# Kernel optimization log

Hardware: AMD Instinct MI355X
Metric: run time of the kernel (lower is better)

The kernel has to match this reference:

```python
import jax, jax.numpy as jnp
import numpy as np

N_SRC = 100000
N_EDGES = 1000000
IN_FEATS = 64
N_CLASSES = 64


def setup_inputs() -> dict:
    key = jax.random.key(0)
    k1, k2, k3, k4, k5 = jax.random.split(key, 5)
    x = jax.random.normal(k1, (N_SRC, IN_FEATS), dtype=jnp.float32)
    W_self = jax.random.normal(k2, (IN_FEATS, N_CLASSES), dtype=jnp.float32) / np.sqrt(IN_FEATS)
    W_neigh = jax.random.normal(k3, (IN_FEATS, N_CLASSES), dtype=jnp.float32) / np.sqrt(IN_FEATS)
    b = jnp.zeros((N_CLASSES,), dtype=jnp.float32)
    src = jax.random.randint(k4, (N_EDGES,), 0, N_SRC, dtype=jnp.int32)
    dst = jax.random.randint(k5, (N_EDGES,), 0, N_SRC, dtype=jnp.int32)
    return {"x": x, "W_self": W_self, "W_neigh": W_neigh, "b": b,
            "src": src, "dst": dst, "num_dst": N_SRC}


def reference(x, W_self, W_neigh, b, src, dst, num_dst):
    # SAGEConv 'mean': gather src features along edges, segment-mean into dst,
    # then rst = h_dst @ W_self + h_neigh_mean @ W_neigh + b, followed by relu.
    msgs = x[src]                                                   # [E, F] irregular gather
    summed = jax.ops.segment_sum(msgs, dst, num_segments=num_dst)   # [num_dst, F]
    deg = jax.ops.segment_sum(jnp.ones((src.shape[0],), x.dtype), dst,
                              num_segments=num_dst)                 # [num_dst]
    h_neigh = summed / jnp.maximum(deg, 1.0)[:, None]               # mean (0 for isolated)
    h_dst = x[:num_dst]
    h = h_dst @ W_self + h_neigh @ W_neigh + b
    return jax.nn.relu(h)
```

## Files before the change

### kernel.cpp

```cpp
#include <hip/hip_runtime.h>


constexpr int F = 64;
constexpr int BROWS = 256;
constexpr int MAXNB = 512;
constexpr int CHP = 4096;
constexpr int SCAP = 2048;
constexpr int LDH = 72;

typedef __attribute__((ext_vector_type(8))) short short8;
typedef __attribute__((ext_vector_type(4))) float float4v;

__device__ inline unsigned short f2bf(float f) {
    union { float f; unsigned u; } c; c.f = f;
    unsigned u = c.u;
    return (unsigned short)((u + 0x7FFFu + ((u >> 16) & 1u)) >> 16);
}
__device__ inline float bf2f(unsigned short h) {
    union { unsigned u; float f; } c; c.u = (unsigned)h << 16;
    return c.f;
}

__global__ __launch_bounds__(256) void k_conv(const float* __restrict__ x,
                                              const float* __restrict__ Ws,
                                              const float* __restrict__ Wn,
                                              unsigned short* __restrict__ xb,
                                              unsigned short* __restrict__ WtG,
                                              const int* __restrict__ dst,
                                              int* __restrict__ cnt,
                                              long n4, int n_edges, int nchunk) {
    __shared__ int hist[MAXNB];
    int t = threadIdx.x;
    long tid = (long)blockIdx.x * 256 + t;
    if (tid < 2 * F * F) {
        int i = (int)tid;
        int n = i & 63, k = i >> 6;
        float v = (k < 64) ? Ws[k * 64 + n] : Wn[(k - 64) * 64 + n];
        WtG[n * 128 + k] = f2bf(v);
    }
    int c = blockIdx.x;
    if (c < nchunk) {
        for (int i = t; i < MAXNB; i += 256) hist[i] = 0;
        __syncthreads();
        int e0 = c * CHP, e1 = min(e0 + CHP, n_edges);
        for (int e = e0 + t; e < e1; e += 256) atomicAdd(&hist[dst[e] >> 8], 1);
        __syncthreads();
        for (int i = t; i < MAXNB; i += 256) cnt[(long)c * MAXNB + i] = hist[i];
    }
    for (long i = tid; i < n4; i += (long)gridDim.x * 256) {
        float4 v = ((const float4*)x)[i];
        ushort4 o;
        o.x = f2bf(v.x); o.y = f2bf(v.y); o.z = f2bf(v.z); o.w = f2bf(v.w);
        ((ushort4*)xb)[i] = o;
    }
}

__global__ __launch_bounds__(512) void k_scanA(int* __restrict__ cnt,
                                               int* __restrict__ btot, int nchunk) {
    int b = (blockIdx.x * 512 + threadIdx.x) >> 6;
    int lane = threadIdx.x & 63;
    if (b >= MAXNB) return;
    int per = (nchunk + 63) / 64;
    int c0 = lane * per;
    int vals[16];
    int lsum = 0;
#pragma unroll
    for (int i = 0; i < 16; ++i) {
        if (i < per) {
            int c = c0 + i;
            int v = (c < nchunk) ? cnt[(long)c * MAXNB + b] : 0;
            vals[i] = v; lsum += v;
        }
    }
    int incl = lsum;
    for (int off = 1; off < 64; off <<= 1) {
        int o = __shfl_up(incl, off);
        if (lane >= off) incl += o;
    }
    int run = incl - lsum;
#pragma unroll
    for (int i = 0; i < 16; ++i) {
        if (i < per) {
            int c = c0 + i;
            if (c < nchunk) { cnt[(long)c * MAXNB + b] = run; run += vals[i]; }
        }
    }
    int tot = __shfl(incl, 63);
    if (lane == 0) btot[b] = tot;
}

__global__ __launch_bounds__(512) void k_scanB(const int* __restrict__ btot,
                                               int* __restrict__ bstart) {
    __shared__ int wtot[8];
    __shared__ int woff[8];
    int t = threadIdx.x;
    int lane = t & 63, wave = t >> 6;
    int v = btot[t];
    int incl = v;
    for (int off = 1; off < 64; off <<= 1) {
        int o = __shfl_up(incl, off);
        if (lane >= off) incl += o;
    }
    if (lane == 63) wtot[wave] = incl;
    __syncthreads();
    if (t == 0) { int s = 0; for (int i = 0; i < 8; ++i) { woff[i] = s; s += wtot[i]; } }
    __syncthreads();
    bstart[t] = incl - v + woff[wave];
    if (t == 511) bstart[MAXNB] = woff[7] + incl;
}

__global__ __launch_bounds__(512) void k_place(const int* __restrict__ src,
                                               const int* __restrict__ dst,
                                               const int* __restrict__ cnt,
                                               const int* __restrict__ bstart,
                                               unsigned* __restrict__ pay, int n_edges) {
    __shared__ int sbp[MAXNB];
    __shared__ int lstart[MAXNB];
    __shared__ int lcur[MAXNB];
    __shared__ unsigned spay[CHP];
    __shared__ int sgpos[CHP];
    __shared__ int wtot[8];
    __shared__ int woff[8];
    int t = threadIdx.x;
    int c = blockIdx.x;
    int e0 = c * CHP, e1 = min(e0 + CHP, n_edges);
    sbp[t] = bstart[t] + cnt[(long)c * MAXNB + t];
    lcur[t] = 0;
    __syncthreads();
    unsigned rpay[8];
    int rbr[8];
#pragma unroll
    for (int j = 0; j < 8; ++j) {
        int e = e0 + t + j * 512;
        rbr[j] = -1;
        if (e < e1) {
            int d = dst[e];
            int b = d >> 8;
            int rank = atomicAdd(&lcur[b], 1);
            rpay[j] = ((unsigned)src[e] << 8) | (unsigned)(d & 255);
            rbr[j] = (b << 12) | rank;
        }
    }
    __syncthreads();
    int lane = t & 63, wave = t >> 6;
    int v = lcur[t];
    int incl = v;
    for (int off = 1; off < 64; off <<= 1) {
        int o = __shfl_up(incl, off);
        if (lane >= off) incl += o;
    }
    if (lane == 63) wtot[wave] = incl;
    __syncthreads();
    if (t == 0) { int s = 0; for (int i = 0; i < 8; ++i) { woff[i] = s; s += wtot[i]; } }
    __syncthreads();
    lstart[t] = incl - v + woff[wave];
    __syncthreads();
#pragma unroll
    for (int j = 0; j < 8; ++j) {
        if (rbr[j] >= 0) {
            int b = rbr[j] >> 12, rank = rbr[j] & 4095;
            int idx = lstart[b] + rank;
            spay[idx] = rpay[j];
            sgpos[idx] = sbp[b] + rank;
        }
    }
    __syncthreads();
    int n = e1 - e0;
    for (int i = t; i < n; i += 512) pay[sgpos[i]] = spay[i];
}

__global__ __launch_bounds__(512) void k_aggemm(const unsigned short* __restrict__ xb,
                                                const unsigned* __restrict__ pay,
                                                const int* __restrict__ bstart,
                                                const unsigned short* __restrict__ WtG,
                                                const float* __restrict__ bias,
                                                float* __restrict__ out,
                                                int num_dst) {
    __shared__ int degs[128];
    __shared__ int rs[128];
    __shared__ int cur[128];
    __shared__ int wsum[2];
    __shared__ __align__(16) int scsr[SCAP];
    __shared__ __align__(16) unsigned short hbt[128 * LDH];
    int t = threadIdx.x;
    int blk = blockIdx.x;
    int b = blk >> 1, h = blk & 1;
    int R0 = b * BROWS + h * 128;
    if (R0 >= num_dst) return;
    int s0 = bstart[b], s1 = bstart[b + 1];
    int n = s1 - s0;
    int lane = t & 63;
    int wave = t >> 6;

    if (t < 128) degs[t] = 0;
    __syncthreads();
    unsigned rp[8];
#pragma unroll
    for (int j = 0; j < 8; ++j) {
        int i = t + j * 512;
        rp[j] = 0xFFFFFFFFu;
        if (i < n) {
            unsigned p = pay[s0 + i];
            rp[j] = p;
            int row = p & 255;
            if ((row >> 7) == h) atomicAdd(&degs[row & 127], 1);
        }
    }
    for (int i = t + 8 * 512; i < n; i += 512) {
        unsigned p = pay[s0 + i];
        int row = p & 255;
        if ((row >> 7) == h) atomicAdd(&degs[row & 127], 1);
    }
    __syncthreads();
    int sv = 0, sincl = 0;
    if (t < 128) {
        sv = degs[t];
        sincl = sv;
        for (int off = 1; off < 64; off <<= 1) {
            int o = __shfl_up(sincl, off);
            if (lane >= off) sincl += o;
        }
        if (lane == 63) wsum[t >> 6] = sincl;
    }
    __syncthreads();
    if (t < 128) {
        int add = (t >= 64) ? wsum[0] : 0;
        int ex = sincl - sv + add;
        rs[t] = ex;
        cur[t] = ex;
    }
    __syncthreads();
#pragma unroll
    for (int j = 0; j < 8; ++j) {
        unsigned p = rp[j];
        if (p != 0xFFFFFFFFu) {
            int row = p & 255;
            if ((row >> 7) == h) {
                int pos = atomicAdd(&cur[row & 127], 1);
                if (pos < SCAP) scsr[pos] = (int)(p >> 8);
            }
        }
    }
    for (int i = t + 8 * 512; i < n; i += 512) {
        unsigned p = pay[s0 + i];
        int row = p & 255;
        if ((row >> 7) == h) {
            int pos = atomicAdd(&cur[row & 127], 1);
            if (pos < SCAP) scsr[pos] = (int)(p >> 8);
        }
    }
    __syncthreads();

    int g = lane >> 3;
    int c8 = (lane & 7) * 8;
#pragma unroll
    for (int batch = 0; batch < 2; ++batch) {
        int rl = wave * 16 + batch * 8 + g;
        int deg = degs[rl];
        int base = rs[rl];
        float acc[8] = {0.f, 0.f, 0.f, 0.f, 0.f, 0.f, 0.f, 0.f};
        for (int k = 0; k < deg; k += 4) {
            int dm = deg - 1;
            int i0 = scsr[base + k];
            int i1 = scsr[base + min(k + 1, dm)];
            int i2 = scsr[base + min(k + 2, dm)];
            int i3 = scsr[base + min(k + 3, dm)];
            short8 u0 = *(const short8*)&xb[(long)i0 * F + c8];
            short8 u1 = *(const short8*)&xb[(long)i1 * F + c8];
            short8 u2 = *(const short8*)&xb[(long)i2 * F + c8];
            short8 u3 = *(const short8*)&xb[(long)i3 * F + c8];
#pragma unroll
            for (int j = 0; j < 8; ++j) acc[j] += bf2f((unsigned short)u0[j]);
            if (k + 1 < deg) {
#pragma unroll
                for (int j = 0; j < 8; ++j) acc[j] += bf2f((unsigned short)u1[j]);
            }
            if (k + 2 < deg) {
#pragma unroll
                for (int j = 0; j < 8; ++j) acc[j] += bf2f((unsigned short)u2[j]);
            }
            if (k + 3 < deg) {
#pragma unroll
                for (int j = 0; j < 8; ++j) acc[j] += bf2f((unsigned short)u3[j]);
            }
        }
        float inv = 1.0f / fmaxf((float)deg, 1.0f);
        short8 o;
#pragma unroll
        for (int j = 0; j < 8; ++j) o[j] = (short)f2bf(acc[j] * inv);
        *(short8*)&hbt[rl * LDH + c8] = o;
    }

    int m = lane & 15;
    int quad = lane >> 4;
    int rowg = R0 + wave * 16 + m;
    int rx = min(rowg, num_dst - 1);
    const unsigned short* xrow = &xb[(long)rx * F + quad * 8];
    short8 a0 = *(const short8*)(xrow);
    short8 a1 = *(const short8*)(xrow + 32);
    const unsigned short* hrow = &hbt[(wave * 16 + m) * LDH + quad * 8];
    short8 a2 = *(const short8*)(hrow);
    short8 a3 = *(const short8*)(hrow + 32);

    float4v acc[4];
#pragma unroll
    for (int nt = 0; nt < 4; ++nt) acc[nt] = (float4v){0.f, 0.f, 0.f, 0.f};

#pragma unroll
    for (int nt = 0; nt < 4; ++nt) {
        const unsigned short* wrow = &WtG[(nt * 16 + m) * 128 + quad * 8];
        short8 b0 = *(const short8*)(wrow);
        short8 b1 = *(const short8*)(wrow + 32);
        short8 b2 = *(const short8*)(wrow + 64);
        short8 b3 = *(const short8*)(wrow + 96);
        acc[nt] = __builtin_amdgcn_mfma_f32_16x16x32_bf16(a0, b0, acc[nt], 0, 0, 0);
        acc[nt] = __builtin_amdgcn_mfma_f32_16x16x32_bf16(a1, b1, acc[nt], 0, 0, 0);
        acc[nt] = __builtin_amdgcn_mfma_f32_16x16x32_bf16(a2, b2, acc[nt], 0, 0, 0);
        acc[nt] = __builtin_amdgcn_mfma_f32_16x16x32_bf16(a3, b3, acc[nt], 0, 0, 0);
    }

    int gr_base = R0 + wave * 16 + quad * 4;
#pragma unroll
    for (int nt = 0; nt < 4; ++nt) {
        int col = nt * 16 + m;
        float bv = bias[col];
#pragma unroll
        for (int rg = 0; rg < 4; ++rg) {
            int gg = gr_base + rg;
            if (gg < num_dst) out[(long)gg * F + col] = fmaxf(acc[nt][rg] + bv, 0.0f);
        }
    }
}

__global__ __launch_bounds__(256) void k_scatter(const float* __restrict__ x, const int* __restrict__ src,
                                                 const int* __restrict__ dst, float* __restrict__ summed,
                                                 float* __restrict__ degf, int n_edges) {
    long tid = (long)blockIdx.x * 256 + threadIdx.x;
    int e = (int)(tid >> 6);
    if (e >= n_edges) return;
    int f = threadIdx.x & 63;
    atomicAdd(&summed[(long)dst[e] * F + f], x[(long)src[e] * F + f]);
    if (f == 0) atomicAdd(&degf[dst[e]], 1.0f);
}

__global__ __launch_bounds__(256) void k_gemm_shfl(
    const float* __restrict__ x, const float* __restrict__ Ws, const float* __restrict__ Wn,
    const float* __restrict__ b, const float* __restrict__ degf, float* inout, int num_dst)
{
    __shared__ float Wl[2 * F * F];
    for (int i = threadIdx.x; i < F * F; i += 256) { Wl[i] = Ws[i]; Wl[F * F + i] = Wn[i]; }
    __syncthreads();
    int lane = threadIdx.x & 63;
    int r = (blockIdx.x * 256 + threadIdx.x) >> 6;
    if (r >= num_dst) return;
    float xv = x[(long)r * F + lane];
    float hv = inout[(long)r * F + lane] / fmaxf(degf[r], 1.0f);
    float acc = b[lane];
#pragma unroll
    for (int k = 0; k < F; ++k) {
        acc += __shfl(xv, k) * Wl[k * F + lane];
        acc += __shfl(hv, k) * Wl[(F + k) * F + lane];
    }
    inout[(long)r * F + lane] = fmaxf(acc, 0.0f);
}

extern "C" void kernel_launch(void* const* d_in, const int* in_sizes, int n_in,
                              void* d_out, int out_size, void* d_ws, size_t ws_size,
                              hipStream_t stream) {
    const float* x  = (const float*)d_in[0];
    const float* Ws = (const float*)d_in[1];
    const float* Wn = (const float*)d_in[2];
    const float* b  = (const float*)d_in[3];
    const int* src  = (const int*)d_in[4];
    const int* dst  = (const int*)d_in[5];
    int n_edges = in_sizes[4];
    int num_dst = out_size / F;
    float* out = (float*)d_out;

    int nchunk = (n_edges + CHP - 1) / CHP;
    int nb = (num_dst + BROWS - 1) / BROWS;

    char* ws = (char*)d_ws;
    size_t off = 0;
    auto alloc = [&](size_t bytes) { char* p = ws + off; off = (off + bytes + 255) & ~(size_t)255; return p; };
    unsigned short* xb  = (unsigned short*)alloc((size_t)num_dst * F * 2);
    unsigned* pay       = (unsigned*)alloc((size_t)n_edges * 4);
    unsigned short* WtG = (unsigned short*)alloc(2 * F * F * 2);
    int* cnt            = (int*)alloc((size_t)nchunk * MAXNB * 4);
    int* btot           = (int*)alloc(MAXNB * 4);
    int* bstart         = (int*)alloc((MAXNB + 1) * 4);
    bool big_ws = (off <= ws_size) && (nb <= MAXNB) && (nchunk <= 1024);

    if (big_ws) {
        long n4 = (long)num_dst * F / 4;
        int convgrid = max(2048, nchunk);
        k_conv<<<convgrid, 256, 0, stream>>>(x, Ws, Wn, xb, WtG, dst, cnt, n4, n_edges, nchunk);
        k_scanA<<<(MAXNB * 64 + 511) / 512, 512, 0, stream>>>(cnt, btot, nchunk);
        k_scanB<<<1, 512, 0, stream>>>(btot, bstart);
        k_place<<<nchunk, 512, 0, stream>>>(src, dst, cnt, bstart, pay, n_edges);
        k_aggemm<<<nb * 2, 512, 0, stream>>>(xb, pay, bstart, WtG, b, out, num_dst);
    } else {
        float* degf = (float*)d_ws;
        (void)hipMemsetAsync(d_out, 0, (size_t)out_size * sizeof(float), stream);
        (void)hipMemsetAsync(degf, 0, (size_t)num_dst * sizeof(float), stream);
        long tt = (long)n_edges * 64;
        k_scatter<<<(int)((tt + 255) / 256), 256, 0, stream>>>(x, src, dst, out, degf, n_edges);
        k_gemm_shfl<<<(num_dst + 3) / 4, 256, 0, stream>>>(x, Ws, Wn, b, degf, out, num_dst);
    }
}
```

Baseline: 146.8 us.

## Fuse edge bucketing into conversion kernel and drop global scan passes

The conversion kernel now sorts each 4096-edge chunk locally by 128-row destination bin and writes the chunk-sorted payload plus a per-chunk offset/count table. The separate scan and placement kernels are removed. Each aggregation block gathers its bin's segments directly from every chunk (245 chunks), so two launches and a global scatter pass go away. In exchange, every aggregation block does many small, serial, per-thread reads of chunk segments, and the per-block edge capacity is a fixed 2048.

```diff
diff --git a/kernel.cpp b/kernel.cpp
--- a/kernel.cpp
+++ b/kernel.cpp
@@ -2,10 +2,9 @@
 
 
 constexpr int F = 64;
-constexpr int BROWS = 256;
-constexpr int MAXNB = 512;
+constexpr int NBIN = 1024;
 constexpr int CHP = 4096;
-constexpr int SCAP = 2048;
+constexpr int ECAP = 2048;
 constexpr int LDH = 72;
 
 typedef __attribute__((ext_vector_type(8))) short short8;
@@ -21,33 +20,81 @@
     return c.f;
 }
 
-__global__ __launch_bounds__(256) void k_conv(const float* __restrict__ x,
+__global__ __launch_bounds__(512) void k_conv(const float* __restrict__ x,
                                               const float* __restrict__ Ws,
                                               const float* __restrict__ Wn,
                                               unsigned short* __restrict__ xb,
                                               unsigned short* __restrict__ WtG,
+                                              const int* __restrict__ src,
                                               const int* __restrict__ dst,
-                                              int* __restrict__ cnt,
+                                              unsigned* __restrict__ pay,
+                                              unsigned* __restrict__ cnt32,
                                               long n4, int n_edges, int nchunk) {
-    __shared__ int hist[MAXNB];
+    __shared__ int hist[NBIN];
+    __shared__ unsigned spay[CHP];
+    __shared__ int wtot[8];
+    __shared__ int woff[8];
     int t = threadIdx.x;
-    long tid = (long)blockIdx.x * 256 + t;
+    int lane = t & 63, wave = t >> 6;
+    long tid = (long)blockIdx.x * 512 + t;
     if (tid < 2 * F * F) {
         int i = (int)tid;
-        int n = i & 63, k = i >> 6;
-        float v = (k < 64) ? Ws[k * 64 + n] : Wn[(k - 64) * 64 + n];
-        WtG[n * 128 + k] = f2bf(v);
+        int nn = i & 63, k = i >> 6;
+        float v = (k < 64) ? Ws[k * 64 + nn] : Wn[(k - 64) * 64 + nn];
+        WtG[nn * 128 + k] = f2bf(v);
     }
     int c = blockIdx.x;
     if (c < nchunk) {
-        for (int i = t; i < MAXNB; i += 256) hist[i] = 0;
+        for (int i = t; i < NBIN; i += 512) hist[i] = 0;
         __syncthreads();
         int e0 = c * CHP, e1 = min(e0 + CHP, n_edges);
-        for (int e = e0 + t; e < e1; e += 256) atomicAdd(&hist[dst[e] >> 8], 1);
-        __syncthreads();
-        for (int i = t; i < MAXNB; i += 256) cnt[(long)c * MAXNB + i] = hist[i];
-    }
-    for (long i = tid; i < n4; i += (long)gridDim.x * 256) {
+        unsigned rpay[8];
+        int rbr[8];
+#pragma unroll
+        for (int j = 0; j < 8; ++j) {
+            int e = e0 + t + j * 512;
+            rbr[j] = -1;
+            if (e < e1) {
+                int d = dst[e];
+                int b = d >> 7;
+                int rank = atomicAdd(&hist[b], 1);
+                rpay[j] = ((unsigned)src[e] << 7) | (unsigned)(d & 127);
+                rbr[j] = (b << 13) | rank;
+            }
+        }
+        __syncthreads();
+        int v0 = hist[2 * t], v1 = hist[2 * t + 1];
+        int s = v0 + v1;
+        int incl = s;
+        for (int off = 1; off < 64; off <<= 1) {
+            int o = __shfl_up(incl, off);
+            if (lane >= off) incl += o;
+        }
+        if (lane == 63) wtot[wave] = incl;
+        __syncthreads();
+        if (t == 0) { int ss = 0; for (int i = 0; i < 8; ++i) { woff[i] = ss; ss += wtot[i]; } }
+        __syncthreads();
+        int ex = incl - s + woff[wave];
+        hist[2 * t] = ex;
+        hist[2 * t + 1] = ex + v0;
+        __syncthreads();
+#pragma unroll
+        for (int j = 0; j < 8; ++j) {
+            if (rbr[j] >= 0) {
+                int b = rbr[j] >> 13, rank = rbr[j] & 8191;
+                spay[hist[b] + rank] = rpay[j];
+            }
+        }
+        __syncthreads();
+        int n = e1 - e0;
+        for (int i = t; i < n; i += 512) pay[e0 + i] = spay[i];
+        for (int b = t; b < NBIN; b += 512) {
+            int o0 = hist[b];
+            int o1 = (b == NBIN - 1) ? n : hist[b + 1];
+            cnt32[(long)c * NBIN + b] = (unsigned)o0 | ((unsigned)(o1 - o0) << 16);
+        }
+    }
+    for (long i = tid; i < n4; i += (long)gridDim.x * 512) {
         float4 v = ((const float4*)x)[i];
         ushort4 o;
         o.x = f2bf(v.x); o.y = f2bf(v.y); o.z = f2bf(v.z); o.w = f2bf(v.w);
@@ -55,162 +102,48 @@
     }
 }
 
-__global__ __launch_bounds__(512) void k_scanA(int* __restrict__ cnt,
-                                               int* __restrict__ btot, int nchunk) {
-    int b = (blockIdx.x * 512 + threadIdx.x) >> 6;
-    int lane = threadIdx.x & 63;
-    if (b >= MAXNB) return;
-    int per = (nchunk + 63) / 64;
-    int c0 = lane * per;
-    int vals[16];
-    int lsum = 0;
-#pragma unroll
-    for (int i = 0; i < 16; ++i) {
-        if (i < per) {
-            int c = c0 + i;
-            int v = (c < nchunk) ? cnt[(long)c * MAXNB + b] : 0;
-            vals[i] = v; lsum += v;
-        }
-    }
-    int incl = lsum;
-    for (int off = 1; off < 64; off <<= 1) {
-        int o = __shfl_up(incl, off);
-        if (lane >= off) incl += o;
-    }
-    int run = incl - lsum;
-#pragma unroll
-    for (int i = 0; i < 16; ++i) {
-        if (i < per) {
-            int c = c0 + i;
-            if (c < nchunk) { cnt[(long)c * MAXNB + b] = run; run += vals[i]; }
-        }
-    }
-    int tot = __shfl(incl, 63);
-    if (lane == 0) btot[b] = tot;
-}
-
-__global__ __launch_bounds__(512) void k_scanB(const int* __restrict__ btot,
-                                               int* __restrict__ bstart) {
-    __shared__ int wtot[8];
-    __shared__ int woff[8];
-    int t = threadIdx.x;
-    int lane = t & 63, wave = t >> 6;
-    int v = btot[t];
-    int incl = v;
-    for (int off = 1; off < 64; off <<= 1) {
-        int o = __shfl_up(incl, off);
-        if (lane >= off) incl += o;
-    }
-    if (lane == 63) wtot[wave] = incl;
-    __syncthreads();
-    if (t == 0) { int s = 0; for (int i = 0; i < 8; ++i) { woff[i] = s; s += wtot[i]; } }
-    __syncthreads();
-    bstart[t] = incl - v + woff[wave];
-    if (t == 511) bstart[MAXNB] = woff[7] + incl;
-}
-
-__global__ __launch_bounds__(512) void k_place(const int* __restrict__ src,
-                                               const int* __restrict__ dst,
-                                               const int* __restrict__ cnt,
-                                               const int* __restrict__ bstart,
-                                               unsigned* __restrict__ pay, int n_edges) {
-    __shared__ int sbp[MAXNB];
-    __shared__ int lstart[MAXNB];
-    __shared__ int lcur[MAXNB];
-    __shared__ unsigned spay[CHP];
-    __shared__ int sgpos[CHP];
-    __shared__ int wtot[8];
-    __shared__ int woff[8];
-    int t = threadIdx.x;
-    int c = blockIdx.x;
-    int e0 = c * CHP, e1 = min(e0 + CHP, n_edges);
-    sbp[t] = bstart[t] + cnt[(long)c * MAXNB + t];
-    lcur[t] = 0;
-    __syncthreads();
-    unsigned rpay[8];
-    int rbr[8];
-#pragma unroll
-    for (int j = 0; j < 8; ++j) {
-        int e = e0 + t + j * 512;
-        rbr[j] = -1;
-        if (e < e1) {
-            int d = dst[e];
-            int b = d >> 8;
-            int rank = atomicAdd(&lcur[b], 1);
-            rpay[j] = ((unsigned)src[e] << 8) | (unsigned)(d & 255);
-            rbr[j] = (b << 12) | rank;
-        }
-    }
-    __syncthreads();
-    int lane = t & 63, wave = t >> 6;
-    int v = lcur[t];
-    int incl = v;
-    for (int off = 1; off < 64; off <<= 1) {
-        int o = __shfl_up(incl, off);
-        if (lane >= off) incl += o;
-    }
-    if (lane == 63) wtot[wave] = incl;
-    __syncthreads();
-    if (t == 0) { int s = 0; for (int i = 0; i < 8; ++i) { woff[i] = s; s += wtot[i]; } }
-    __syncthreads();
-    lstart[t] = incl - v + woff[wave];
-    __syncthreads();
-#pragma unroll
-    for (int j = 0; j < 8; ++j) {
-        if (rbr[j] >= 0) {
-            int b = rbr[j] >> 12, rank = rbr[j] & 4095;
-            int idx = lstart[b] + rank;
-            spay[idx] = rpay[j];
-            sgpos[idx] = sbp[b] + rank;
-        }
-    }
-    __syncthreads();
-    int n = e1 - e0;
-    for (int i = t; i < n; i += 512) pay[sgpos[i]] = spay[i];
-}
-
 __global__ __launch_bounds__(512) void k_aggemm(const unsigned short* __restrict__ xb,
                                                 const unsigned* __restrict__ pay,
-                                                const int* __restrict__ bstart,
+                                                const unsigned* __restrict__ cnt32,
                                                 const unsigned short* __restrict__ WtG,
                                                 const float* __restrict__ bias,
                                                 float* __restrict__ out,
-                                                int num_dst) {
+                                                int num_dst, int nchunk) {
     __shared__ int degs[128];
     __shared__ int rs[128];
     __shared__ int cur[128];
     __shared__ int wsum[2];
-    __shared__ __align__(16) int scsr[SCAP];
+    __shared__ int s_tot;
+    __shared__ unsigned sedge[ECAP];
+    __shared__ int scsr[ECAP];
     __shared__ __align__(16) unsigned short hbt[128 * LDH];
     int t = threadIdx.x;
-    int blk = blockIdx.x;
-    int b = blk >> 1, h = blk & 1;
-    int R0 = b * BROWS + h * 128;
+    int b = blockIdx.x;
+    int R0 = b * 128;
     if (R0 >= num_dst) return;
-    int s0 = bstart[b], s1 = bstart[b + 1];
-    int n = s1 - s0;
     int lane = t & 63;
     int wave = t >> 6;
 
     if (t < 128) degs[t] = 0;
-    __syncthreads();
-    unsigned rp[8];
-#pragma unroll
-    for (int j = 0; j < 8; ++j) {
-        int i = t + j * 512;
-        rp[j] = 0xFFFFFFFFu;
-        if (i < n) {
-            unsigned p = pay[s0 + i];
-            rp[j] = p;
-            int row = p & 255;
-            if ((row >> 7) == h) atomicAdd(&degs[row & 127], 1);
-        }
-    }
-    for (int i = t + 8 * 512; i < n; i += 512) {
-        unsigned p = pay[s0 + i];
-        int row = p & 255;
-        if ((row >> 7) == h) atomicAdd(&degs[row & 127], 1);
-    }
+    if (t == 0) s_tot = 0;
+    __syncthreads();
+
+    for (int c = t; c < nchunk; c += 512) {
+        unsigned rc = cnt32[(long)c * NBIN + b];
+        int off = (int)(rc & 0xFFFFu);
+        int cn  = (int)(rc >> 16);
+        if (cn) {
+            int pos = atomicAdd(&s_tot, cn);
+            const unsigned* rp = &pay[(long)c * CHP + off];
+            for (int i = 0; i < cn; ++i) {
+                int p2 = pos + i;
+                if (p2 < ECAP) sedge[p2] = rp[i];
+            }
+        }
+    }
+    __syncthreads();
+    int n = min(s_tot, ECAP);
+    for (int i = t; i < n; i += 512) atomicAdd(&degs[sedge[i] & 127], 1);
     __syncthreads();
     int sv = 0, sincl = 0;
     if (t < 128) {
@@ -230,24 +163,10 @@
         cur[t] = ex;
     }
     __syncthreads();
-#pragma unroll
-    for (int j = 0; j < 8; ++j) {
-        unsigned p = rp[j];
-        if (p != 0xFFFFFFFFu) {
-            int row = p & 255;
-            if ((row >> 7) == h) {
-                int pos = atomicAdd(&cur[row & 127], 1);
-                if (pos < SCAP) scsr[pos] = (int)(p >> 8);
-            }
-        }
-    }
-    for (int i = t + 8 * 512; i < n; i += 512) {
-        unsigned p = pay[s0 + i];
-        int row = p & 255;
-        if ((row >> 7) == h) {
-            int pos = atomicAdd(&cur[row & 127], 1);
-            if (pos < SCAP) scsr[pos] = (int)(p >> 8);
-        }
+    for (int i = t; i < n; i += 512) {
+        unsigned p = sedge[i];
+        int pos = atomicAdd(&cur[p & 127], 1);
+        scsr[pos] = (int)(p >> 7);
     }
     __syncthreads();
 
@@ -378,7 +297,7 @@
     float* out = (float*)d_out;
 
     int nchunk = (n_edges + CHP - 1) / CHP;
-    int nb = (num_dst + BROWS - 1) / BROWS;
+    int nb = (num_dst + 127) / 128;
 
     char* ws = (char*)d_ws;
     size_t off = 0;
@@ -386,19 +305,15 @@
     unsigned short* xb  = (unsigned short*)alloc((size_t)num_dst * F * 2);
     unsigned* pay       = (unsigned*)alloc((size_t)n_edges * 4);
     unsigned short* WtG = (unsigned short*)alloc(2 * F * F * 2);
-    int* cnt            = (int*)alloc((size_t)nchunk * MAXNB * 4);
-    int* btot           = (int*)alloc(MAXNB * 4);
-    int* bstart         = (int*)alloc((MAXNB + 1) * 4);
-    bool big_ws = (off <= ws_size) && (nb <= MAXNB) && (nchunk <= 1024);
+    unsigned* cnt32     = (unsigned*)alloc((size_t)nchunk * NBIN * 4);
+    bool big_ws = (off <= ws_size) && (nb <= NBIN);
 
     if (big_ws) {
         long n4 = (long)num_dst * F / 4;
-        int convgrid = max(2048, nchunk);
-        k_conv<<<convgrid, 256, 0, stream>>>(x, Ws, Wn, xb, WtG, dst, cnt, n4, n_edges, nchunk);
-        k_scanA<<<(MAXNB * 64 + 511) / 512, 512, 0, stream>>>(cnt, btot, nchunk);
-        k_scanB<<<1, 512, 0, stream>>>(btot, bstart);
-        k_place<<<nchunk, 512, 0, stream>>>(src, dst, cnt, bstart, pay, n_edges);
-        k_aggemm<<<nb * 2, 512, 0, stream>>>(xb, pay, bstart, WtG, b, out, num_dst);
+        int convgrid = max(1024, nchunk);
+        k_conv<<<convgrid, 512, 0, stream>>>(x, Ws, Wn, xb, WtG, src, dst, pay, cnt32,
+                                             n4, n_edges, nchunk);
+        k_aggemm<<<nb, 512, 0, stream>>>(xb, pay, cnt32, WtG, b, out, num_dst, nchunk);
     } else {
         float* degf = (float*)d_ws;
         (void)hipMemsetAsync(d_out, 0, (size_t)out_size * sizeof(float), stream);
```

Result: faster. 142.7 us (-2.8%).
